# Kernel tuning notes

Hardware: AMD Instinct MI355X
Metric: run time of the kernel (lower is better)

Reference implementation:

```python
import jax, jax.numpy as jnp
import numpy as np

N = 50000      # nodes
E = 800000     # edges
IN = 64        # in_channels
HID = 16       # hidden_channels
HEADS = 4
HC = HID * HEADS  # 64 == IN, so all 3 layers share in-dim 64
EDIM = 16
L = 3
G = 2000       # graphs
BN_EPS = 1e-5


def setup_inputs() -> dict:
    key = jax.random.key(0)
    ks = jax.random.split(key, 24)
    inp = {
        "x": jax.random.normal(ks[0], (N, IN), jnp.float32),
        "edge_index": jax.random.randint(ks[1], (2, E), 0, N, jnp.int64),
        "edge_attr": jax.random.normal(ks[2], (E, EDIM), jnp.float32),
        "batch": jnp.sort(jax.random.randint(ks[3], (N,), 0, G, jnp.int64)),
    }
    s = 0.05
    # stacked per-layer TransformerConv params (all layers have in-dim 64)
    inp["Wq"] = jax.random.normal(ks[4], (L, HC, HC), jnp.float32) * s
    inp["bq"] = jnp.zeros((L, HC), jnp.float32)
    inp["Wk"] = jax.random.normal(ks[5], (L, HC, HC), jnp.float32) * s
    inp["bk"] = jnp.zeros((L, HC), jnp.float32)
    inp["Wv"] = jax.random.normal(ks[6], (L, HC, HC), jnp.float32) * s
    inp["bv"] = jnp.zeros((L, HC), jnp.float32)
    inp["We"] = jax.random.normal(ks[7], (L, EDIM, HC), jnp.float32) * s  # lin_edge, no bias
    inp["Ws"] = jax.random.normal(ks[8], (L, HC, HC), jnp.float32) * s   # lin_skip
    inp["bs"] = jnp.zeros((L, HC), jnp.float32)
    # BatchNorm1d (eval mode) per layer
    inp["bn_g"] = jnp.ones((L, HC), jnp.float32)
    inp["bn_b"] = jnp.zeros((L, HC), jnp.float32)
    inp["bn_m"] = jax.random.normal(ks[9], (L, HC), jnp.float32) * 0.01
    inp["bn_v"] = 0.5 + jax.random.uniform(ks[10], (L, HC), jnp.float32)
    # head MLP
    inp["fc1_w"] = jax.random.normal(ks[11], (HC, HID), jnp.float32) * s
    inp["fc1_b"] = jnp.zeros((HID,), jnp.float32)
    inp["fc2_w"] = jax.random.normal(ks[12], (HID, 1), jnp.float32) * s
    inp["fc2_b"] = jnp.zeros((1,), jnp.float32)
    return inp


def _segment_softmax(logits, seg, n):
    # logits: [E, H]; softmax over edges sharing the same target node
    m = jax.ops.segment_max(logits, seg, num_segments=n)       # [N, H]
    ex = jnp.exp(logits - m[seg])
    den = jax.ops.segment_sum(ex, seg, num_segments=n)         # [N, H]
    return ex / den[seg]


def _transformer_conv(x, src, dst, edge_attr, Wq, bq, Wk, bk, Wv, bv, We, Ws, bs):
    n = x.shape[0]
    q = (x @ Wq + bq).reshape(n, HEADS, HID)[dst]              # [E, H, C]
    e_emb = (edge_attr @ We).reshape(-1, HEADS, HID)           # [E, H, C]
    k = (x @ Wk + bk).reshape(n, HEADS, HID)[src] + e_emb
    v = (x @ Wv + bv).reshape(n, HEADS, HID)[src] + e_emb
    logits = jnp.sum(q * k, axis=-1) / jnp.sqrt(jnp.asarray(HID, x.dtype))  # [E, H]
    alpha = _segment_softmax(logits, dst, n)
    agg = jax.ops.segment_sum(alpha[..., None] * v, dst, num_segments=n)    # [N, H, C]
    return agg.reshape(n, HC) + x @ Ws + bs


def reference(x, edge_index, edge_attr, batch, Wq, bq, Wk, bk, Wv, bv, We, Ws, bs,
              bn_g, bn_b, bn_m, bn_v, fc1_w, fc1_b, fc2_w, fc2_b):
    src, dst = edge_index[0], edge_index[1]
    for l in range(Wq.shape[0]):
        x = _transformer_conv(x, src, dst, edge_attr,
                              Wq[l], bq[l], Wk[l], bk[l], Wv[l], bv[l],
                              We[l], Ws[l], bs[l])
        x = jax.nn.relu((x - bn_m[l]) * jax.lax.rsqrt(bn_v[l] + BN_EPS) * bn_g[l] + bn_b[l])
        # dropout is identity in eval / p given at init
    counts = jax.ops.segment_sum(jnp.ones((x.shape[0],), x.dtype), batch, num_segments=G)
    pooled = jax.ops.segment_sum(x, batch, num_segments=G) / jnp.maximum(counts, 1.0)[:, None]
    h = jax.nn.relu(pooled @ fc1_w + fc1_b)
    return h @ fc2_w + fc2_b
```

## Files before the change

### kernel.cpp

```cpp
#include <hip/hip_runtime.h>
#include <math.h>

#define N_NODES 50000
#define N_EDGES 800000
#define HC 64
#define HID 16
#define EDIM 16
#define NGRAPH 2000
#define BN_EPS 1e-5f
#define QKVS_NODES 32
#define SCAN_NBLK ((N_NODES + 255) / 256)

__device__ inline unsigned short f2bf(float f) {
    union { float f; unsigned u; } v; v.f = f;
    unsigned r = v.u + 0x7fffu + ((v.u >> 16) & 1u);
    return (unsigned short)(r >> 16);
}
__device__ inline float4 bf4_to_f4(uint2 r) {
    float4 o;
    o.x = __uint_as_float(r.x << 16);
    o.y = __uint_as_float(r.x & 0xffff0000u);
    o.z = __uint_as_float(r.y << 16);
    o.w = __uint_as_float(r.y & 0xffff0000u);
    return o;
}

__global__ void count_deg(const int* __restrict__ ei, int* __restrict__ deg) {
    int e = blockIdx.x * blockDim.x + threadIdx.x;
    if (e < N_EDGES) atomicAdd(&deg[ei[N_EDGES + e]], 1);
}

__global__ __launch_bounds__(256) void scan1(const int* __restrict__ deg, int* __restrict__ bsum) {
    __shared__ int s[256];
    int tid = threadIdx.x;
    int i = blockIdx.x * 256 + tid;
    s[tid] = (i < N_NODES) ? deg[i] : 0;
    __syncthreads();
    for (int d = 128; d > 0; d >>= 1) {
        if (tid < d) s[tid] += s[tid + d];
        __syncthreads();
    }
    if (tid == 0) bsum[blockIdx.x] = s[0];
}

__global__ __launch_bounds__(256) void scan2(const int* __restrict__ bsum, int* __restrict__ boff) {
    __shared__ int s[256];
    int tid = threadIdx.x;
    int v = (tid < SCAN_NBLK) ? bsum[tid] : 0;
    s[tid] = v;
    __syncthreads();
    for (int d = 1; d < 256; d <<= 1) {
        int t = (tid >= d) ? s[tid - d] : 0;
        __syncthreads();
        s[tid] += t;
        __syncthreads();
    }
    boff[tid] = s[tid] - v;
}

__global__ __launch_bounds__(256) void scan3(const int* __restrict__ deg, const int* __restrict__ boff,
                                             int* __restrict__ row_ptr, int* __restrict__ nxt) {
    __shared__ int s[256];
    int tid = threadIdx.x;
    int i = blockIdx.x * 256 + tid;
    int v = (i < N_NODES) ? deg[i] : 0;
    s[tid] = v;
    __syncthreads();
    for (int d = 1; d < 256; d <<= 1) {
        int t = (tid >= d) ? s[tid - d] : 0;
        __syncthreads();
        s[tid] += t;
        __syncthreads();
    }
    int excl = s[tid] - v + boff[blockIdx.x];
    if (i < N_NODES) { row_ptr[i] = excl; nxt[i] = excl; }
    if (i == 0) row_ptr[N_NODES] = N_EDGES;
}

__global__ void scatter_edges(const int* __restrict__ ei, int* __restrict__ next_ptr,
                              int2* __restrict__ se_s) {
    int e = blockIdx.x * blockDim.x + threadIdx.x;
    if (e < N_EDGES) {
        int d = ei[N_EDGES + e];
        int p = atomicAdd(&next_ptr[d], 1);
        se_s[p] = make_int2(ei[e], e);
    }
}

__global__ __launch_bounds__(256) void qkvs_kernel(
    const float* __restrict__ x,
    const float* __restrict__ Wq, const float* __restrict__ bq,
    const float* __restrict__ Wk, const float* __restrict__ bk,
    const float* __restrict__ Wv, const float* __restrict__ bv,
    const float* __restrict__ Ws, const float* __restrict__ bs,
    const float* __restrict__ We,
    float* __restrict__ Qo, unsigned short* __restrict__ KVo, float* __restrict__ So,
    float* __restrict__ qwe_buf) {
    __shared__ float xs[QKVS_NODES][HC];
    int tid = threadIdx.x;
    int n0 = blockIdx.x * QKVS_NODES;
    for (int c = tid; c < QKVS_NODES * HC / 4; c += 256) {
        int row = c >> 4, col4 = c & 15;
        int n = n0 + row;
        float4 v = (n < N_NODES) ? ((const float4*)(x + (size_t)n * HC))[col4]
                                 : make_float4(0.f, 0.f, 0.f, 0.f);
        ((float4*)&xs[row][0])[col4] = v;
    }
    __syncthreads();
    int sel = tid >> 6;
    int j = tid & 63;
    const float* W; const float* B;
    if (sel == 0)      { W = Wq; B = bq; }
    else if (sel == 1) { W = Wk; B = bk; }
    else if (sel == 2) { W = Wv; B = bv; }
    else               { W = Ws; B = bs; }
    float bias = B[j];
    float acc[QKVS_NODES];
#pragma unroll
    for (int n = 0; n < QKVS_NODES; n++) acc[n] = bias;
    for (int i4 = 0; i4 < HC / 4; i4++) {
        float w0 = W[(i4 * 4 + 0) * HC + j];
        float w1 = W[(i4 * 4 + 1) * HC + j];
        float w2 = W[(i4 * 4 + 2) * HC + j];
        float w3 = W[(i4 * 4 + 3) * HC + j];
#pragma unroll
        for (int n = 0; n < QKVS_NODES; n++) {
            float4 xv = ((const float4*)&xs[n][0])[i4];
            acc[n] = fmaf(xv.x, w0, acc[n]);
            acc[n] = fmaf(xv.y, w1, acc[n]);
            acc[n] = fmaf(xv.z, w2, acc[n]);
            acc[n] = fmaf(xv.w, w3, acc[n]);
        }
    }
    if (sel == 0 || sel == 3) {
        float* Out = (sel == 0) ? Qo : So;
#pragma unroll
        for (int n = 0; n < QKVS_NODES; n++) {
            int node = n0 + n;
            if (node < N_NODES) Out[(size_t)node * HC + j] = acc[n];
        }
    } else {
        int off = (sel == 1) ? 0 : HC;
#pragma unroll
        for (int n = 0; n < QKVS_NODES; n++) {
            int node = n0 + n;
            if (node < N_NODES) KVo[(size_t)node * 2 * HC + off + j] = f2bf(acc[n]);
        }
    }

    __syncthreads();
    if (sel == 0) {
#pragma unroll
        for (int n = 0; n < QKVS_NODES; n++) xs[n][j] = acc[n];
    }
    __syncthreads();
    {
        int h2 = j >> 4, jj = j & 15;
        float4 wv0 = *(const float4*)(We + jj * HC + h2 * 16 + 0);
        float4 wv1 = *(const float4*)(We + jj * HC + h2 * 16 + 4);
        float4 wv2 = *(const float4*)(We + jj * HC + h2 * 16 + 8);
        float4 wv3 = *(const float4*)(We + jj * HC + h2 * 16 + 12);
#pragma unroll
        for (int n = 0; n < 8; n++) {
            int nn = sel * 8 + n;
            float4 q0 = *(const float4*)&xs[nn][h2 * 16 + 0];
            float4 q1 = *(const float4*)&xs[nn][h2 * 16 + 4];
            float4 q2 = *(const float4*)&xs[nn][h2 * 16 + 8];
            float4 q3 = *(const float4*)&xs[nn][h2 * 16 + 12];
            float s = q0.x * wv0.x + q0.y * wv0.y + q0.z * wv0.z + q0.w * wv0.w
                    + q1.x * wv1.x + q1.y * wv1.y + q1.z * wv1.z + q1.w * wv1.w
                    + q2.x * wv2.x + q2.y * wv2.y + q2.z * wv2.z + q2.w * wv2.w
                    + q3.x * wv3.x + q3.y * wv3.y + q3.z * wv3.z + q3.w * wv3.w;
            int node = n0 + nn;
            if (node < N_NODES) qwe_buf[(size_t)node * HC + j] = s;
        }
    }
}

__global__ __launch_bounds__(256) void attn_kernel(
    const float* __restrict__ Qf, const float* __restrict__ Qwe,
    const unsigned short* __restrict__ KV, const float* __restrict__ Sf,
    const int* __restrict__ row_ptr, const int2* __restrict__ se_s,
    const float* __restrict__ edge_attr, const float* __restrict__ We,
    const float* __restrict__ bng, const float* __restrict__ bnb,
    const float* __restrict__ bnm, const float* __restrict__ bnv,
    float* __restrict__ x_out) {
    __shared__ float we_s[EDIM * HC];
    int tid = threadIdx.x;
    for (int c = tid; c < EDIM * HC / 4; c += 256)
        ((float4*)we_s)[c] = ((const float4*)We)[c];
    __syncthreads();

    int lane = tid & 63;
    int wave = tid >> 6;
    int half = lane >> 5;
    int node = blockIdx.x * 8 + wave * 2 + half;
    int sub = (lane >> 4) & 1;
    int pos = lane & 15;
    int h = pos >> 2;
    int eaIdx = pos & 3;
    int rbeg = row_ptr[node], rend = row_ptr[node + 1];

    float4 q4 = ((const float4*)(Qf + (size_t)node * HC))[pos];
    float4 qwe = ((const float4*)(Qwe + (size_t)node * HC))[pos];

    float m = -1e30f, den = 0.f;
    float4 acc = make_float4(0.f, 0.f, 0.f, 0.f);
    float4 aea = make_float4(0.f, 0.f, 0.f, 0.f);

    auto proc = [&](float4 k4, float4 ea4) -> float {
        float dot = q4.x * k4.x + q4.y * k4.y + q4.z * k4.z + q4.w * k4.w
                  + qwe.x * ea4.x + qwe.y * ea4.y + qwe.z * ea4.z + qwe.w * ea4.w;
        dot += __shfl_xor(dot, 1);
        dot += __shfl_xor(dot, 2);
        float logit = dot * 0.25f;
        float mn = fmaxf(m, logit);
        float corr = __expf(m - mn);
        float p = __expf(logit - mn);
        den = den * corr + p;
        acc.x *= corr; acc.y *= corr; acc.z *= corr; acc.w *= corr;
        aea.x *= corr; aea.y *= corr; aea.z *= corr; aea.w *= corr;
        m = mn;
        return p;
    };
    auto accum = [&](float p, const float4& v, const float4& ea) {
        acc.x = fmaf(p, v.x, acc.x); acc.y = fmaf(p, v.y, acc.y);
        acc.z = fmaf(p, v.z, acc.z); acc.w = fmaf(p, v.w, acc.w);
        aea.x = fmaf(p, ea.x, aea.x); aea.y = fmaf(p, ea.y, aea.y);
        aea.z = fmaf(p, ea.z, aea.z); aea.w = fmaf(p, ea.w, aea.w);
    };

    int j = rbeg + sub;
    for (; j + 2 < rend; j += 4) {
        int2 se0 = se_s[j];
        int2 se1 = se_s[j + 2];
        const unsigned short* kv0 = KV + (size_t)se0.x * 2 * HC;
        const unsigned short* kv1 = KV + (size_t)se1.x * 2 * HC;
        uint2 k0r = *(const uint2*)(kv0 + pos * 4);
        uint2 v0r = *(const uint2*)(kv0 + HC + pos * 4);
        uint2 k1r = *(const uint2*)(kv1 + pos * 4);
        uint2 v1r = *(const uint2*)(kv1 + HC + pos * 4);
        float4 ea0 = ((const float4*)(edge_attr + (size_t)se0.y * EDIM))[eaIdx];
        float4 ea1 = ((const float4*)(edge_attr + (size_t)se1.y * EDIM))[eaIdx];
        float4 k0 = bf4_to_f4(k0r), v0 = bf4_to_f4(v0r);
        float4 k1 = bf4_to_f4(k1r), v1 = bf4_to_f4(v1r);
        float p0 = proc(k0, ea0);
        accum(p0, v0, ea0);
        float p1 = proc(k1, ea1);
        accum(p1, v1, ea1);
    }
    if (j < rend) {
        int2 se0 = se_s[j];
        const unsigned short* kv0 = KV + (size_t)se0.x * 2 * HC;
        uint2 k0r = *(const uint2*)(kv0 + pos * 4);
        uint2 v0r = *(const uint2*)(kv0 + HC + pos * 4);
        float4 ea0 = ((const float4*)(edge_attr + (size_t)se0.y * EDIM))[eaIdx];
        float4 k0 = bf4_to_f4(k0r), v0 = bf4_to_f4(v0r);
        float p0 = proc(k0, ea0);
        accum(p0, v0, ea0);
    }

    {
        float m2 = __shfl_xor(m, 16);
        float d2 = __shfl_xor(den, 16);
        float ax = __shfl_xor(acc.x, 16), ay = __shfl_xor(acc.y, 16);
        float az = __shfl_xor(acc.z, 16), aw = __shfl_xor(acc.w, 16);
        float bx = __shfl_xor(aea.x, 16), by = __shfl_xor(aea.y, 16);
        float bz = __shfl_xor(aea.z, 16), bw = __shfl_xor(aea.w, 16);
        float mn = fmaxf(m, m2);
        float c1 = __expf(m - mn), c2 = __expf(m2 - mn);
        den = den * c1 + d2 * c2;
        acc.x = acc.x * c1 + ax * c2; acc.y = acc.y * c1 + ay * c2;
        acc.z = acc.z * c1 + az * c2; acc.w = acc.w * c1 + aw * c2;
        aea.x = aea.x * c1 + bx * c2; aea.y = aea.y * c1 + by * c2;
        aea.z = aea.z * c1 + bz * c2; aea.w = aea.w * c1 + bw * c2;
        m = mn;
    }

    float4 e4 = make_float4(0.f, 0.f, 0.f, 0.f);
#pragma unroll
    for (int jg = 0; jg < 4; jg++) {
        int sl = (lane & 32) | (h * 4 + jg);
        float a0 = __shfl(aea.x, sl), a1 = __shfl(aea.y, sl);
        float a2 = __shfl(aea.z, sl), a3 = __shfl(aea.w, sl);
        float4 w0 = *(const float4*)(we_s + (jg * 4 + 0) * HC + pos * 4);
        float4 w1 = *(const float4*)(we_s + (jg * 4 + 1) * HC + pos * 4);
        float4 w2 = *(const float4*)(we_s + (jg * 4 + 2) * HC + pos * 4);
        float4 w3 = *(const float4*)(we_s + (jg * 4 + 3) * HC + pos * 4);
        e4.x += a0 * w0.x + a1 * w1.x + a2 * w2.x + a3 * w3.x;
        e4.y += a0 * w0.y + a1 * w1.y + a2 * w2.y + a3 * w3.y;
        e4.z += a0 * w0.z + a1 * w1.z + a2 * w2.z + a3 * w3.z;
        e4.w += a0 * w0.w + a1 * w1.w + a2 * w2.w + a3 * w3.w;
    }

    float inv = (rend > rbeg) ? 1.f / den : 0.f;
    float4 sk = ((const float4*)(Sf + (size_t)node * HC))[pos];
    float4 o = make_float4((acc.x + e4.x) * inv + sk.x, (acc.y + e4.y) * inv + sk.y,
                           (acc.z + e4.z) * inv + sk.z, (acc.w + e4.w) * inv + sk.w);
    float4 g4 = ((const float4*)bng)[pos];
    float4 b4 = ((const float4*)bnb)[pos];
    float4 m4 = ((const float4*)bnm)[pos];
    float4 vv4 = ((const float4*)bnv)[pos];
    o.x = fmaxf((o.x - m4.x) * rsqrtf(vv4.x + BN_EPS) * g4.x + b4.x, 0.f);
    o.y = fmaxf((o.y - m4.y) * rsqrtf(vv4.y + BN_EPS) * g4.y + b4.y, 0.f);
    o.z = fmaxf((o.z - m4.z) * rsqrtf(vv4.z + BN_EPS) * g4.z + b4.z, 0.f);
    o.w = fmaxf((o.w - m4.w) * rsqrtf(vv4.w + BN_EPS) * g4.w + b4.w, 0.f);
    if (sub == 0) ((float4*)(x_out + (size_t)node * HC))[pos] = o;
}

__global__ __launch_bounds__(256) void pool_head(
    const float* __restrict__ x, const int* __restrict__ batch,
    const float* __restrict__ fc1_w, const float* __restrict__ fc1_b,
    const float* __restrict__ fc2_w, const float* __restrict__ fc2_b,
    float* __restrict__ out) {
    __shared__ float ps[4][HC];
    int q = threadIdx.x >> 6;
    int lane = threadIdx.x & 63;
    int g = blockIdx.x * 4 + q;
    int lo = 0, hi = N_NODES;
    while (lo < hi) { int mid = (lo + hi) >> 1; if (batch[mid] < g) lo = mid + 1; else hi = mid; }
    int beg = lo;
    lo = 0; hi = N_NODES;
    while (lo < hi) { int mid = (lo + hi) >> 1; if (batch[mid] < g + 1) lo = mid + 1; else hi = mid; }
    int end = lo;
    float s = 0.f;
    for (int i = beg; i < end; i++) s += x[(size_t)i * HC + lane];
    float inv = (end > beg) ? 1.f / (float)(end - beg) : 1.f;
    ps[q][lane] = s * inv;
    __syncthreads();
    float o = 0.f;
    if (lane < HID) {
        float a = fc1_b[lane];
#pragma unroll
        for (int i = 0; i < HC; i++) a = fmaf(ps[q][i], fc1_w[i * HID + lane], a);
        o = fmaxf(a, 0.f) * fc2_w[lane];
    }
    o += __shfl_xor(o, 1);
    o += __shfl_xor(o, 2);
    o += __shfl_xor(o, 4);
    o += __shfl_xor(o, 8);
    if (lane == 0) out[g] = o + fc2_b[0];
}

extern "C" void kernel_launch(void* const* d_in, const int* in_sizes, int n_in,
                              void* d_out, int out_size, void* d_ws, size_t ws_size,
                              hipStream_t stream) {
    const float* x         = (const float*)d_in[0];
    const int*   ei        = (const int*)d_in[1];
    const float* edge_attr = (const float*)d_in[2];
    const int*   batch     = (const int*)d_in[3];
    const float* Wq = (const float*)d_in[4];  const float* bq = (const float*)d_in[5];
    const float* Wk = (const float*)d_in[6];  const float* bk = (const float*)d_in[7];
    const float* Wv = (const float*)d_in[8];  const float* bv = (const float*)d_in[9];
    const float* We = (const float*)d_in[10];
    const float* Ws = (const float*)d_in[11]; const float* bs = (const float*)d_in[12];
    const float* bng = (const float*)d_in[13]; const float* bnb = (const float*)d_in[14];
    const float* bnm = (const float*)d_in[15]; const float* bnv = (const float*)d_in[16];
    const float* fc1_w = (const float*)d_in[17]; const float* fc1_b = (const float*)d_in[18];
    const float* fc2_w = (const float*)d_in[19]; const float* fc2_b = (const float*)d_in[20];
    float* out = (float*)d_out;

    char* wp = (char*)d_ws;
    auto alloc = [&](size_t b) { void* p = (void*)wp; wp += (b + 255) & ~(size_t)255; return p; };
    float* xA      = (float*)alloc((size_t)N_NODES * HC * 4);
    float* xB      = (float*)alloc((size_t)N_NODES * HC * 4);
    float* Qb      = (float*)alloc((size_t)N_NODES * HC * 4);
    float* Sb      = (float*)alloc((size_t)N_NODES * HC * 4);
    unsigned short* KV = (unsigned short*)alloc((size_t)N_NODES * 2 * HC * 2);
    float* qweb    = (float*)alloc((size_t)N_NODES * HC * 4);
    int*   deg     = (int*)alloc((size_t)N_NODES * 4);
    int*   row_ptr = (int*)alloc((size_t)(N_NODES + 1) * 4);
    int*   nxt     = (int*)alloc((size_t)N_NODES * 4);
    int*   bsum    = (int*)alloc((size_t)256 * 4);
    int*   boff    = (int*)alloc((size_t)256 * 4);
    int2*  se_s    = (int2*)alloc((size_t)N_EDGES * 8);

    (void)hipMemsetAsync(deg, 0, (size_t)N_NODES * 4, stream);

    count_deg<<<(N_EDGES + 255) / 256, 256, 0, stream>>>(ei, deg);
    scan1<<<SCAN_NBLK, 256, 0, stream>>>(deg, bsum);
    scan2<<<1, 256, 0, stream>>>(bsum, boff);
    scan3<<<SCAN_NBLK, 256, 0, stream>>>(deg, boff, row_ptr, nxt);
    scatter_edges<<<(N_EDGES + 255) / 256, 256, 0, stream>>>(ei, nxt, se_s);

    const float* xin = x;
    float* bufs[2] = {xA, xB};
    for (int l = 0; l < 3; l++) {
        float* xout = bufs[l & 1];
        qkvs_kernel<<<(N_NODES + QKVS_NODES - 1) / QKVS_NODES, 256, 0, stream>>>(
            xin, Wq + l * HC * HC, bq + l * HC, Wk + l * HC * HC, bk + l * HC,
            Wv + l * HC * HC, bv + l * HC, Ws + l * HC * HC, bs + l * HC,
            We + l * EDIM * HC, Qb, KV, Sb, qweb);
        attn_kernel<<<N_NODES / 8, 256, 0, stream>>>(
            Qb, qweb, KV, Sb, row_ptr, se_s, edge_attr, We + l * EDIM * HC,
            bng + l * HC, bnb + l * HC, bnm + l * HC, bnv + l * HC, xout);
        xin = xout;
    }
    pool_head<<<NGRAPH / 4, 256, 0, stream>>>(xin, batch, fc1_w, fc1_b, fc2_w, fc2_b, out);
}
```

Baseline: 544.5 us.

## Fuse CSR build into a single persistent kernel with grid barriers

Replaces the five CSR-construction kernels (degree count, three scan stages, edge scatter) with one persistent kernel of 256 blocks that uses atomic spin grid barriers between phases. This removes four kernel launch boundaries and their drain gaps. The barrier counter is zeroed by the existing memset. The risks are spin-wait overhead and fewer threads for the atomic-heavy edge loops, and correctness depends on all 256 blocks being co-resident.

```diff
diff --git a/kernel.cpp b/kernel.cpp
--- a/kernel.cpp
+++ b/kernel.cpp
@@ -9,7 +9,8 @@
 #define NGRAPH 2000
 #define BN_EPS 1e-5f
 #define QKVS_NODES 32
-#define SCAN_NBLK ((N_NODES + 255) / 256)
+#define CSR_NBLK 256
+#define CSR_GSZ (CSR_NBLK * 256)
 
 __device__ inline unsigned short f2bf(float f) {
     union { float f; unsigned u; } v; v.f = f;
@@ -25,28 +26,35 @@
     return o;
 }
 
-__global__ void count_deg(const int* __restrict__ ei, int* __restrict__ deg) {
-    int e = blockIdx.x * blockDim.x + threadIdx.x;
-    if (e < N_EDGES) atomicAdd(&deg[ei[N_EDGES + e]], 1);
-}
-
-__global__ __launch_bounds__(256) void scan1(const int* __restrict__ deg, int* __restrict__ bsum) {
+__device__ inline void grid_bar(int* bar, int slot) {
+    __threadfence();
+    __syncthreads();
+    if (threadIdx.x == 0) {
+        atomicAdd(&bar[slot], 1);
+        while (atomicAdd(&bar[slot], 0) < CSR_NBLK) { }
+        __threadfence();
+    }
+    __syncthreads();
+}
+
+__global__ __launch_bounds__(256) void csr_build(
+    const int* __restrict__ ei,
+    int* __restrict__ deg,
+    int* __restrict__ bar,
+    int* __restrict__ bsum, int* __restrict__ boff,
+    int* __restrict__ row_ptr, int* __restrict__ nxt,
+    int2* __restrict__ se_s) {
+    const int tid = threadIdx.x;
+    const int bid = blockIdx.x;
+    const int gid = bid * 256 + tid;
     __shared__ int s[256];
-    int tid = threadIdx.x;
-    int i = blockIdx.x * 256 + tid;
-    s[tid] = (i < N_NODES) ? deg[i] : 0;
-    __syncthreads();
-    for (int d = 128; d > 0; d >>= 1) {
-        if (tid < d) s[tid] += s[tid + d];
-        __syncthreads();
-    }
-    if (tid == 0) bsum[blockIdx.x] = s[0];
-}
-
-__global__ __launch_bounds__(256) void scan2(const int* __restrict__ bsum, int* __restrict__ boff) {
-    __shared__ int s[256];
-    int tid = threadIdx.x;
-    int v = (tid < SCAN_NBLK) ? bsum[tid] : 0;
+    __shared__ int boff_s;
+
+    for (int e = gid; e < N_EDGES; e += CSR_GSZ)
+        atomicAdd(&deg[ei[N_EDGES + e]], 1);
+    grid_bar(bar, 0);
+
+    int v = (gid < N_NODES) ? atomicAdd(&deg[gid], 0) : 0;
     s[tid] = v;
     __syncthreads();
     for (int d = 1; d < 256; d <<= 1) {
@@ -55,34 +63,37 @@
         s[tid] += t;
         __syncthreads();
     }
-    boff[tid] = s[tid] - v;
-}
-
-__global__ __launch_bounds__(256) void scan3(const int* __restrict__ deg, const int* __restrict__ boff,
-                                             int* __restrict__ row_ptr, int* __restrict__ nxt) {
-    __shared__ int s[256];
-    int tid = threadIdx.x;
-    int i = blockIdx.x * 256 + tid;
-    int v = (i < N_NODES) ? deg[i] : 0;
-    s[tid] = v;
-    __syncthreads();
-    for (int d = 1; d < 256; d <<= 1) {
-        int t = (tid >= d) ? s[tid - d] : 0;
+    int excl = s[tid] - v;
+    if (tid == 255) atomicExch(&bsum[bid], s[255]);
+    grid_bar(bar, 1);
+
+    if (bid == 0) {
+        int v2 = atomicAdd(&bsum[tid], 0);
+        s[tid] = v2;
         __syncthreads();
-        s[tid] += t;
-        __syncthreads();
-    }
-    int excl = s[tid] - v + boff[blockIdx.x];
-    if (i < N_NODES) { row_ptr[i] = excl; nxt[i] = excl; }
-    if (i == 0) row_ptr[N_NODES] = N_EDGES;
-}
-
-__global__ void scatter_edges(const int* __restrict__ ei, int* __restrict__ next_ptr,
-                              int2* __restrict__ se_s) {
-    int e = blockIdx.x * blockDim.x + threadIdx.x;
-    if (e < N_EDGES) {
+        for (int d = 1; d < 256; d <<= 1) {
+            int t = (tid >= d) ? s[tid - d] : 0;
+            __syncthreads();
+            s[tid] += t;
+            __syncthreads();
+        }
+        atomicExch(&boff[tid], s[tid] - v2);
+    }
+    grid_bar(bar, 2);
+
+    if (tid == 0) boff_s = atomicAdd(&boff[bid], 0);
+    __syncthreads();
+    if (gid < N_NODES) {
+        int rp = excl + boff_s;
+        row_ptr[gid] = rp;
+        atomicExch(&nxt[gid], rp);
+    }
+    if (gid == 0) row_ptr[N_NODES] = N_EDGES;
+    grid_bar(bar, 3);
+
+    for (int e = gid; e < N_EDGES; e += CSR_GSZ) {
         int d = ei[N_EDGES + e];
-        int p = atomicAdd(&next_ptr[d], 1);
+        int p = atomicAdd(&nxt[d], 1);
         se_s[p] = make_int2(ei[e], e);
     }
 }
@@ -368,20 +379,18 @@
     float* Sb      = (float*)alloc((size_t)N_NODES * HC * 4);
     unsigned short* KV = (unsigned short*)alloc((size_t)N_NODES * 2 * HC * 2);
     float* qweb    = (float*)alloc((size_t)N_NODES * HC * 4);
-    int*   deg     = (int*)alloc((size_t)N_NODES * 4);
+    int*   degbar  = (int*)alloc((size_t)(N_NODES + 16) * 4);
+    int*   deg     = degbar;
+    int*   bar     = degbar + N_NODES;
     int*   row_ptr = (int*)alloc((size_t)(N_NODES + 1) * 4);
     int*   nxt     = (int*)alloc((size_t)N_NODES * 4);
     int*   bsum    = (int*)alloc((size_t)256 * 4);
     int*   boff    = (int*)alloc((size_t)256 * 4);
     int2*  se_s    = (int2*)alloc((size_t)N_EDGES * 8);
 
-    (void)hipMemsetAsync(deg, 0, (size_t)N_NODES * 4, stream);
-
-    count_deg<<<(N_EDGES + 255) / 256, 256, 0, stream>>>(ei, deg);
-    scan1<<<SCAN_NBLK, 256, 0, stream>>>(deg, bsum);
-    scan2<<<1, 256, 0, stream>>>(bsum, boff);
-    scan3<<<SCAN_NBLK, 256, 0, stream>>>(deg, boff, row_ptr, nxt);
-    scatter_edges<<<(N_EDGES + 255) / 256, 256, 0, stream>>>(ei, nxt, se_s);
+    (void)hipMemsetAsync(degbar, 0, (size_t)(N_NODES + 16) * 4, stream);
+
+    csr_build<<<CSR_NBLK, 256, 0, stream>>>(ei, deg, bar, bsum, boff, row_ptr, nxt, se_s);
 
     const float* xin = x;
     float* bufs[2] = {xA, xB};
```

New measurement: 643.7 us. +18.2%, slower.
